# Kernel optimization log

Measured on AMD Instinct MI355X. Metric: run time of the kernel, lower is better.

The kernel has to match this reference:

```python
import jax, jax.numpy as jnp
import numpy as np

N = 100000   # nodes
E = 1600000  # edges
C = 128      # hidden_channels
L = 3        # num_layers
V = 128      # embedding vocab


def setup_inputs() -> dict:
    key = jax.random.key(0)
    ks = jax.random.split(key, 10)
    s = 1.0 / np.sqrt(C)
    return {
        "x_idx": jax.random.randint(ks[0], (N,), 0, V),
        "edge_index": jax.random.randint(ks[1], (2, E), 0, N),
        "edge_weight": jax.random.uniform(ks[2], (E,), dtype=jnp.float32),
        "emb": jax.random.normal(ks[3], (V, C), dtype=jnp.float32),
        "conv_w": jax.random.uniform(ks[4], (L, C, C), minval=-s, maxval=s, dtype=jnp.float32),
        "conv_b": jnp.zeros((L, C), dtype=jnp.float32),
        "lin1_w": jax.random.uniform(ks[5], (C, C), minval=-s, maxval=s, dtype=jnp.float32),
        "lin1_b": jnp.zeros((C,), dtype=jnp.float32),
        "lin2_w": jax.random.uniform(ks[6], (C, 2), minval=-s, maxval=s, dtype=jnp.float32),
        "lin2_b": jnp.zeros((2,), dtype=jnp.float32),
    }


def reference(x_idx, edge_index, edge_weight, emb, conv_w, conv_b,
              lin1_w, lin1_b, lin2_w, lin2_b):
    # GCNConv (PyG): add self-loops (weight 1), symmetric normalization
    row, col = edge_index[0], edge_index[1]
    loop = jnp.arange(N)
    r = jnp.concatenate([row, loop])
    c = jnp.concatenate([col, loop])
    w = jnp.concatenate([edge_weight, jnp.ones((N,), edge_weight.dtype)])
    deg = jax.ops.segment_sum(w, c, num_segments=N)            # [N]
    dinv = jnp.where(deg > 0, jax.lax.rsqrt(deg), 0.0)
    norm = dinv[r] * w * dinv[c]                               # [E+N]

    x = emb[x_idx]                                             # [N, C]
    for i in range(L):
        xw = x @ conv_w[i]                                     # [N, C]
        # message: norm * xw[src], aggregate at dst
        x = jax.ops.segment_sum(norm[:, None] * xw[r], c, num_segments=N) + conv_b[i]
        if i < L - 1:
            x = jax.nn.relu(x)  # dropout is identity in eval mode

    x = jax.nn.relu(x @ lin1_w + lin1_b)
    return x @ lin2_w + lin2_b                                 # [N, 2]
```

## Files before the change

kernel.cpp:

```cpp
#include <hip/hip_runtime.h>
#include <hip/hip_fp16.h>

#define NN 100000
#define NE 1600000
#define CC 128
#define NB_SCAN 391
#define CAP 1900032

typedef _Float16 f16x8 __attribute__((ext_vector_type(8)));
typedef float    f32x4 __attribute__((ext_vector_type(4)));

__global__ void k_init(int* cnt) {
    int i = blockIdx.x * 256 + threadIdx.x;
    if (i < NN) cnt[i] = 0;
}

__global__ void k_count(const int* __restrict__ ei, int* cnt, int* loc) {
    int e = blockIdx.x * 256 + threadIdx.x;
    if (e < NE) {
        int c = ei[NE + e];
        loc[e] = atomicAdd(&cnt[c], 1);
    }
}

__global__ void k_scan1(const int* __restrict__ cnt, int* rowptr, int* bsum) {
    __shared__ int s[256];
    int t = threadIdx.x;
    int i = blockIdx.x * 256 + t;
    int v = (i < NN) ? ((cnt[i] + 3) & ~3) : 0;
    s[t] = v; __syncthreads();
    for (int off = 1; off < 256; off <<= 1) {
        int x = (t >= off) ? s[t - off] : 0;
        __syncthreads();
        s[t] += x;
        __syncthreads();
    }
    if (i < NN) rowptr[i] = s[t] - v;
    if (t == 255) bsum[blockIdx.x] = s[255];
}

__global__ void k_scan2(const int* __restrict__ bsum, int* boff) {
    __shared__ int s[512];
    int t = threadIdx.x;
    int v = (t < NB_SCAN) ? bsum[t] : 0;
    s[t] = v; __syncthreads();
    for (int off = 1; off < 512; off <<= 1) {
        int x = (t >= off) ? s[t - off] : 0;
        __syncthreads();
        s[t] += x;
        __syncthreads();
    }
    if (t < NB_SCAN) boff[t] = s[t] - v;
}

__global__ void k_scan3(int* rowptr, const int* __restrict__ boff,
                        const int* __restrict__ cnt) {
    int i = blockIdx.x * 256 + threadIdx.x;
    if (i < NN) {
        rowptr[i] += boff[i >> 8];
        if (i == NN - 1) rowptr[NN] = rowptr[i] + ((cnt[i] + 3) & ~3);
    }
}

__global__ void k_scatter(const int* __restrict__ ei, const float* __restrict__ ew,
                          const int* __restrict__ loc, const int* __restrict__ rowptr,
                          int2* __restrict__ csr) {
    int e = blockIdx.x * 256 + threadIdx.x;
    if (e < NE) {
        int c = ei[NE + e];
        int pos = rowptr[c] + loc[e];
        csr[pos] = make_int2(ei[e], __float_as_int(ew[e]));
    }
}

__global__ void k_degdinv(const int* __restrict__ rowptr, const int2* __restrict__ csr,
                          float* __restrict__ dinv) {
    int v = blockIdx.x * 256 + threadIdx.x;
    if (v < NN) {
        int b = rowptr[v], e = rowptr[v + 1];
        float s = 1.f;
        for (int i = b; i < e; i++) s += __int_as_float(csr[i].y);
        dinv[v] = rsqrtf(s);
    }
}

__global__ void k_mkcsr0(const int2* __restrict__ csr, const int* __restrict__ xidx,
                         const float* __restrict__ dinv, int2* __restrict__ csr0) {
    int e = blockIdx.x * 256 + threadIdx.x;
    if (e < CAP) {
        int2 c = csr[e];
        csr0[e] = make_int2(xidx[c.x],
                            __float_as_int(__int_as_float(c.y) * dinv[c.x]));
    }
}

__global__ void k_wcvt(const float* __restrict__ conv_w, const float* __restrict__ lin1_w,
                       _Float16* __restrict__ wt) {
    int t = blockIdx.x * 256 + threadIdx.x;
    int l = t >> 14, r = t & 16383;
    int j = r >> 7, k = r & 127;
    const float* src = (l < 2) ? (conv_w + (l + 1) * 16384) : lin1_w;
    wt[l * 16384 + j * 128 + k] = (_Float16)src[k * 128 + j];
}

__global__ void k_embw(const float* __restrict__ emb, const float* __restrict__ w0,
                       __half2* __restrict__ ewh) {
    int t = blockIdx.x * 256 + threadIdx.x;
    int i = t >> 6, jp = t & 63;
    int j0 = jp * 2;
    float a0 = 0.f, a1 = 0.f;
    for (int k = 0; k < 128; k++) {
        float e = emb[i * 128 + k];
        a0 = fmaf(e, w0[k * 128 + j0], a0);
        a1 = fmaf(e, w0[k * 128 + j0 + 1], a1);
    }
    ewh[t] = __floats2half2_rn(a0, a1);
}

template <int SELF_TABLE, int RELU>
__device__ __forceinline__ void agg_core(const _Float16* __restrict__ src16,
                                         const int2* __restrict__ csr,
                                         const int* __restrict__ rowptr,
                                         const int* __restrict__ xidx,
                                         const float* __restrict__ dinv,
                                         const float* __restrict__ bias,
                                         _Float16* __restrict__ xout) {
    int wave = threadIdx.x >> 6, lane = threadIdx.x & 63;
    int g = lane >> 4, sub = lane & 15;
    int v = blockIdx.x * 4 + wave;
    if (v >= NN) return;
    int beg = rowptr[v], end = rowptr[v + 1];
    float acc[8];
#pragma unroll
    for (int i = 0; i < 8; i++) acc[i] = 0.f;
    int e = beg;
    while (e + 8 <= end) {
        int2 c0 = csr[e + g];
        int2 c1 = csr[e + 4 + g];
        f16x8 t0 = *reinterpret_cast<const f16x8*>(&src16[(size_t)c0.x * 128 + sub * 8]);
        f16x8 t1 = *reinterpret_cast<const f16x8*>(&src16[(size_t)c1.x * 128 + sub * 8]);
        float w0 = __int_as_float(c0.y), w1 = __int_as_float(c1.y);
#pragma unroll
        for (int i = 0; i < 8; i++) acc[i] = fmaf(w0, (float)t0[i], acc[i]);
#pragma unroll
        for (int i = 0; i < 8; i++) acc[i] = fmaf(w1, (float)t1[i], acc[i]);
        e += 8;
    }
    if (e < end) {
        int2 c0 = csr[e + g];
        f16x8 t0 = *reinterpret_cast<const f16x8*>(&src16[(size_t)c0.x * 128 + sub * 8]);
        float w0 = __int_as_float(c0.y);
#pragma unroll
        for (int i = 0; i < 8; i++) acc[i] = fmaf(w0, (float)t0[i], acc[i]);
    }
#pragma unroll
    for (int i = 0; i < 8; i++) {
        acc[i] += __shfl_down(acc[i], 32);
        acc[i] += __shfl_down(acc[i], 16);
    }
    if (g == 0) {
        float dv = dinv[v];
        size_t selfoff = SELF_TABLE ? (size_t)xidx[v] * 128 : (size_t)v * 128;
        f16x8 sf = *reinterpret_cast<const f16x8*>(&src16[selfoff + sub * 8]);
        float4 b0 = reinterpret_cast<const float4*>(bias)[sub * 2];
        float4 b1 = reinterpret_cast<const float4*>(bias)[sub * 2 + 1];
        float bb[8] = {b0.x, b0.y, b0.z, b0.w, b1.x, b1.y, b1.z, b1.w};
        f16x8 o;
#pragma unroll
        for (int i = 0; i < 8; i++) {
            float self = SELF_TABLE ? dv * (float)sf[i] : (float)sf[i];
            float r = fmaf(dv, acc[i] + self, bb[i]);
            if (RELU) r = fmaxf(r, 0.f);
            o[i] = (_Float16)r;
        }
        *reinterpret_cast<f16x8*>(&xout[(size_t)v * 128 + sub * 8]) = o;
    }
}

__global__ void k_agg0(const int2* __restrict__ csr0, const int* __restrict__ rowptr,
                       const int* __restrict__ xidx, const float* __restrict__ dinv,
                       const _Float16* __restrict__ ewh, const float* __restrict__ bias,
                       _Float16* __restrict__ xout) {
    agg_core<1, 1>(ewh, csr0, rowptr, xidx, dinv, bias, xout);
}

__global__ void k_agg_r(const _Float16* __restrict__ y, const int* __restrict__ rowptr,
                        const int2* __restrict__ csr, const float* __restrict__ dinv,
                        const float* __restrict__ bias, _Float16* __restrict__ xout) {
    agg_core<0, 1>(y, csr, rowptr, nullptr, dinv, bias, xout);
}

__global__ void k_agg_n(const _Float16* __restrict__ y, const int* __restrict__ rowptr,
                        const int2* __restrict__ csr, const float* __restrict__ dinv,
                        const float* __restrict__ bias, _Float16* __restrict__ xout) {
    agg_core<0, 0>(y, csr, rowptr, nullptr, dinv, bias, xout);
}

template <int MODE>
__global__ __launch_bounds__(256) void k_mgemm(const _Float16* __restrict__ A,
                                               const _Float16* __restrict__ Wt,
                                               const float* __restrict__ dinv,
                                               const float* __restrict__ bias,
                                               _Float16* __restrict__ yout,
                                               const float* __restrict__ w2,
                                               const float* __restrict__ b2,
                                               float* __restrict__ outf) {
    int wid = threadIdx.x >> 6, lane = threadIdx.x & 63;
    int lc = lane & 15, lg = lane >> 4;
    int arow = blockIdx.x * 64 + wid * 16 + lc;
    bool rok = arow < NN;

    f32x4 acc[8];
#pragma unroll
    for (int j = 0; j < 8; j++) acc[j] = (f32x4){0.f, 0.f, 0.f, 0.f};

#pragma unroll
    for (int kc = 0; kc < 4; kc++) {
        int k0 = kc * 32 + lg * 8;
        f16x8 a = {0, 0, 0, 0, 0, 0, 0, 0};
        if (rok) a = *reinterpret_cast<const f16x8*>(&A[arow * 128 + k0]);
#pragma unroll
        for (int j = 0; j < 8; j++) {
            f16x8 b = *reinterpret_cast<const f16x8*>(&Wt[(j * 16 + lc) * 128 + k0]);
            acc[j] = __builtin_amdgcn_mfma_f32_16x16x32_f16(a, b, acc[j], 0, 0, 0);
        }
    }

    int orow0 = blockIdx.x * 64 + wid * 16 + lg * 4;
    if (MODE == 0) {
        float dv[4];
#pragma unroll
        for (int r = 0; r < 4; r++)
            dv[r] = (orow0 + r < NN) ? dinv[orow0 + r] : 0.f;
#pragma unroll
        for (int j = 0; j < 8; j++) {
#pragma unroll
            for (int r = 0; r < 4; r++) {
                int orow = orow0 + r;
                if (orow < NN)
                    yout[orow * 128 + j * 16 + lc] = (_Float16)(dv[r] * acc[j][r]);
            }
        }
    } else {
        float bj[8], w0j[8], w1j[8];
#pragma unroll
        for (int j = 0; j < 8; j++) {
            int c = j * 16 + lc;
            bj[j] = bias[c];
            w0j[j] = w2[c * 2 + 0];
            w1j[j] = w2[c * 2 + 1];
        }
        float bb0 = b2[0], bb1 = b2[1];
#pragma unroll
        for (int r = 0; r < 4; r++) {
            float p0 = 0.f, p1 = 0.f;
#pragma unroll
            for (int j = 0; j < 8; j++) {
                float h = fmaxf(acc[j][r] + bj[j], 0.f);
                p0 = fmaf(h, w0j[j], p0);
                p1 = fmaf(h, w1j[j], p1);
            }
#pragma unroll
            for (int m = 1; m < 16; m <<= 1) {
                p0 += __shfl_xor(p0, m);
                p1 += __shfl_xor(p1, m);
            }
            int orow = orow0 + r;
            if (lc == 0 && orow < NN)
                *reinterpret_cast<float2*>(&outf[orow * 2]) =
                    make_float2(p0 + bb0, p1 + bb1);
        }
    }
}

extern "C" void kernel_launch(void* const* d_in, const int* in_sizes, int n_in,
                              void* d_out, int out_size, void* d_ws, size_t ws_size,
                              hipStream_t stream) {
    const int*   x_idx  = (const int*)d_in[0];
    const int*   ei     = (const int*)d_in[1];
    const float* ew     = (const float*)d_in[2];
    const float* emb    = (const float*)d_in[3];
    const float* conv_w = (const float*)d_in[4];
    const float* conv_b = (const float*)d_in[5];
    const float* lin1_w = (const float*)d_in[6];
    const float* lin1_b = (const float*)d_in[7];
    const float* lin2_w = (const float*)d_in[8];
    const float* lin2_b = (const float*)d_in[9];
    float* out = (float*)d_out;

    char* ws = (char*)d_ws;
    size_t off = 0;
    auto alloc = [&](size_t bytes) -> void* {
        void* p = ws + off;
        off += (bytes + 255) & ~(size_t)255;
        return p;
    };
    float*    dinv   = (float*)alloc(NN * 4);
    int*      cnt    = (int*)alloc(NN * 4);
    int*      rowptr = (int*)alloc((NN + 1) * 4);
    int*      bsum   = (int*)alloc(512 * 4);
    int*      boff   = (int*)alloc(512 * 4);
    int*      loc    = (int*)alloc((size_t)NE * 4);
    int2*     csr    = (int2*)alloc((size_t)CAP * 8);
    int2*     csr0   = (int2*)alloc((size_t)CAP * 8);
    _Float16* ewh    = (_Float16*)alloc(128 * 128 * 2);
    _Float16* wt     = (_Float16*)alloc(3 * 128 * 128 * 2);
    _Float16* xbuf   = (_Float16*)alloc((size_t)NN * CC * 2);
    _Float16* ybuf   = (_Float16*)alloc((size_t)NN * CC * 2);
    (void)ws_size;

    const int NBn = (NN + 255) / 256;
    const int NBe = (NE + 255) / 256;
    const int NBc = CAP / 256;
    const int NBg = (NN + 63) / 64;

    hipMemsetAsync(csr, 0, (size_t)CAP * 8, stream);
    k_init<<<NBn, 256, 0, stream>>>(cnt);
    k_count<<<NBe, 256, 0, stream>>>(ei, cnt, loc);
    k_scan1<<<NB_SCAN, 256, 0, stream>>>(cnt, rowptr, bsum);
    k_scan2<<<1, 512, 0, stream>>>(bsum, boff);
    k_scan3<<<NBn, 256, 0, stream>>>(rowptr, boff, cnt);
    k_scatter<<<NBe, 256, 0, stream>>>(ei, ew, loc, rowptr, csr);
    k_degdinv<<<NBn, 256, 0, stream>>>(rowptr, csr, dinv);
    k_mkcsr0<<<NBc, 256, 0, stream>>>(csr, x_idx, dinv, csr0);
    k_wcvt<<<192, 256, 0, stream>>>(conv_w, lin1_w, wt);

    k_embw<<<32, 256, 0, stream>>>(emb, conv_w, (__half2*)ewh);
    k_agg0<<<NN / 4, 256, 0, stream>>>(csr0, rowptr, x_idx, dinv, ewh,
                                       conv_b + 0 * CC, xbuf);
    k_mgemm<0><<<NBg, 256, 0, stream>>>(xbuf, wt + 0 * 16384, dinv, nullptr, ybuf,
                                        nullptr, nullptr, nullptr);
    k_agg_r<<<NN / 4, 256, 0, stream>>>(ybuf, rowptr, csr, dinv, conv_b + 1 * CC, xbuf);
    k_mgemm<0><<<NBg, 256, 0, stream>>>(xbuf, wt + 1 * 16384, dinv, nullptr, ybuf,
                                        nullptr, nullptr, nullptr);
    k_agg_n<<<NN / 4, 256, 0, stream>>>(ybuf, rowptr, csr, dinv, conv_b + 2 * CC, xbuf);
    k_mgemm<1><<<NBg, 256, 0, stream>>>(xbuf, wt + 2 * 16384, dinv, lin1_b, nullptr,
                                        lin2_w, lin2_b, out);
}
```

Before: 432.9 us.

## Build CSR with two-level binned counting sort in shared memory

Replaces the global-atomic per-node count plus scatter CSR build with a two-pass binned sort. Edges are first histogrammed into 128-node bins per block, then scattered into bin-contiguous buffers, and finally locally sorted in shared memory per bin, which also computes rowptr and dinv. Because rows are no longer padded to multiples of 4, the aggregation tail loop now handles partial groups with masked loads. This removes the memset, the global atomics and the separate degree pass, at the cost of extra intermediate buffers and a reliance on each bin fitting within MAXB shared-memory entries.

```diff
diff --git a/kernel.cpp b/kernel.cpp
--- a/kernel.cpp
+++ b/kernel.cpp
@@ -4,30 +4,36 @@
 #define NN 100000
 #define NE 1600000
 #define CC 128
-#define NB_SCAN 391
-#define CAP 1900032
+#define NBIN 782
+#define BPW 128
+#define MAXB 2560
+#define NHB 256
+#define EPB 6250
 
 typedef _Float16 f16x8 __attribute__((ext_vector_type(8)));
 typedef float    f32x4 __attribute__((ext_vector_type(4)));
 
-__global__ void k_init(int* cnt) {
-    int i = blockIdx.x * 256 + threadIdx.x;
-    if (i < NN) cnt[i] = 0;
-}
-
-__global__ void k_count(const int* __restrict__ ei, int* cnt, int* loc) {
-    int e = blockIdx.x * 256 + threadIdx.x;
-    if (e < NE) {
-        int c = ei[NE + e];
-        loc[e] = atomicAdd(&cnt[c], 1);
-    }
-}
-
-__global__ void k_scan1(const int* __restrict__ cnt, int* rowptr, int* bsum) {
+__global__ __launch_bounds__(256) void k_hist(const int* __restrict__ ei,
+                                              int* __restrict__ hist) {
+    __shared__ int h[NBIN];
+    for (int i = threadIdx.x; i < NBIN; i += 256) h[i] = 0;
+    __syncthreads();
+    int base = blockIdx.x * EPB;
+    for (int i = threadIdx.x; i < EPB; i += 256) {
+        int d = ei[NE + base + i];
+        atomicAdd(&h[d >> 7], 1);
+    }
+    __syncthreads();
+    for (int i = threadIdx.x; i < NBIN; i += 256)
+        hist[blockIdx.x * NBIN + i] = h[i];
+}
+
+__global__ __launch_bounds__(256) void k_scanA(const int* __restrict__ hist,
+                                               int* __restrict__ blockBase,
+                                               int* __restrict__ binTotal) {
     __shared__ int s[256];
-    int t = threadIdx.x;
-    int i = blockIdx.x * 256 + t;
-    int v = (i < NN) ? ((cnt[i] + 3) & ~3) : 0;
+    int bin = blockIdx.x, t = threadIdx.x;
+    int v = hist[t * NBIN + bin];
     s[t] = v; __syncthreads();
     for (int off = 1; off < 256; off <<= 1) {
         int x = (t >= off) ? s[t - off] : 0;
@@ -35,59 +41,103 @@
         s[t] += x;
         __syncthreads();
     }
-    if (i < NN) rowptr[i] = s[t] - v;
-    if (t == 255) bsum[blockIdx.x] = s[255];
-}
-
-__global__ void k_scan2(const int* __restrict__ bsum, int* boff) {
-    __shared__ int s[512];
+    blockBase[t * NBIN + bin] = s[t] - v;
+    if (t == 255) binTotal[bin] = s[255];
+}
+
+__global__ __launch_bounds__(1024) void k_scanB(const int* __restrict__ binTotal,
+                                                int* __restrict__ binStart) {
+    __shared__ int s[1024];
     int t = threadIdx.x;
-    int v = (t < NB_SCAN) ? bsum[t] : 0;
+    int v = (t < NBIN) ? binTotal[t] : 0;
     s[t] = v; __syncthreads();
-    for (int off = 1; off < 512; off <<= 1) {
+    for (int off = 1; off < 1024; off <<= 1) {
         int x = (t >= off) ? s[t - off] : 0;
         __syncthreads();
         s[t] += x;
         __syncthreads();
     }
-    if (t < NB_SCAN) boff[t] = s[t] - v;
-}
-
-__global__ void k_scan3(int* rowptr, const int* __restrict__ boff,
-                        const int* __restrict__ cnt) {
-    int i = blockIdx.x * 256 + threadIdx.x;
-    if (i < NN) {
-        rowptr[i] += boff[i >> 8];
-        if (i == NN - 1) rowptr[NN] = rowptr[i] + ((cnt[i] + 3) & ~3);
-    }
-}
-
-__global__ void k_scatter(const int* __restrict__ ei, const float* __restrict__ ew,
-                          const int* __restrict__ loc, const int* __restrict__ rowptr,
-                          int2* __restrict__ csr) {
-    int e = blockIdx.x * 256 + threadIdx.x;
-    if (e < NE) {
-        int c = ei[NE + e];
-        int pos = rowptr[c] + loc[e];
-        csr[pos] = make_int2(ei[e], __float_as_int(ew[e]));
-    }
-}
-
-__global__ void k_degdinv(const int* __restrict__ rowptr, const int2* __restrict__ csr,
-                          float* __restrict__ dinv) {
-    int v = blockIdx.x * 256 + threadIdx.x;
-    if (v < NN) {
-        int b = rowptr[v], e = rowptr[v + 1];
-        float s = 1.f;
-        for (int i = b; i < e; i++) s += __int_as_float(csr[i].y);
-        dinv[v] = rsqrtf(s);
-    }
+    if (t < NBIN) binStart[t] = s[t] - v;
+    if (t == 1023) binStart[NBIN] = s[1023];
+}
+
+__global__ __launch_bounds__(256) void k_pass2(const int* __restrict__ ei,
+                                               const float* __restrict__ ew,
+                                               const int* __restrict__ binStart,
+                                               const int* __restrict__ blockBase,
+                                               int2* __restrict__ pay,
+                                               unsigned char* __restrict__ key) {
+    __shared__ int cur[NBIN];
+    int blk = blockIdx.x;
+    for (int i = threadIdx.x; i < NBIN; i += 256)
+        cur[i] = binStart[i] + blockBase[blk * NBIN + i];
+    __syncthreads();
+    int base = blk * EPB;
+    for (int i = threadIdx.x; i < EPB; i += 256) {
+        int e = base + i;
+        int d = ei[NE + e];
+        int src = ei[e];
+        float w = ew[e];
+        int pos = atomicAdd(&cur[d >> 7], 1);
+        pay[pos] = make_int2(src, __float_as_int(w));
+        key[pos] = (unsigned char)(d & 127);
+    }
+}
+
+__global__ __launch_bounds__(256) void k_pass3(const int* __restrict__ binStart,
+                                               const int2* __restrict__ pay,
+                                               const unsigned char* __restrict__ key,
+                                               int2* __restrict__ csr,
+                                               int* __restrict__ rowptr,
+                                               float* __restrict__ dinv) {
+    __shared__ int2 sp[MAXB];
+    __shared__ unsigned char sk[MAXB];
+    __shared__ int hist[BPW], excl[BPW], cur[BPW];
+    __shared__ float degw[BPW];
+    int b = blockIdx.x, t = threadIdx.x;
+    int s0 = binStart[b], s1 = binStart[b + 1];
+    int n = s1 - s0;
+    if (t < BPW) { hist[t] = 0; degw[t] = 0.f; }
+    __syncthreads();
+    for (int i = t; i < n; i += 256) {
+        int2 p = pay[s0 + i];
+        unsigned char k = key[s0 + i];
+        sp[i] = p; sk[i] = k;
+        atomicAdd(&hist[k], 1);
+    }
+    __syncthreads();
+    if (t < BPW) excl[t] = hist[t];
+    __syncthreads();
+    for (int off = 1; off < BPW; off <<= 1) {
+        int x = (t < BPW && t >= off) ? excl[t - off] : 0;
+        __syncthreads();
+        if (t < BPW) excl[t] += x;
+        __syncthreads();
+    }
+    if (t < BPW) {
+        int ex = excl[t] - hist[t];
+        excl[t] = ex;
+        cur[t] = ex;
+    }
+    __syncthreads();
+    int node0 = b * BPW;
+    if (t < BPW && node0 + t < NN) rowptr[node0 + t] = s0 + excl[t];
+    if (b == NBIN - 1 && t == 0) rowptr[NN] = NE;
+    for (int i = t; i < n; i += 256) {
+        int2 p = sp[i];
+        unsigned char k = sk[i];
+        int pos = atomicAdd(&cur[k], 1);
+        csr[s0 + pos] = p;
+        atomicAdd(&degw[k], __int_as_float(p.y));
+    }
+    __syncthreads();
+    if (t < BPW && node0 + t < NN) dinv[node0 + t] = rsqrtf(1.f + degw[t]);
 }
 
 __global__ void k_mkcsr0(const int2* __restrict__ csr, const int* __restrict__ xidx,
                          const float* __restrict__ dinv, int2* __restrict__ csr0) {
     int e = blockIdx.x * 256 + threadIdx.x;
-    if (e < CAP) {
+    if (e < NE) {
         int2 c = csr[e];
         csr0[e] = make_int2(xidx[c.x],
                             __float_as_int(__int_as_float(c.y) * dinv[c.x]));
@@ -146,10 +196,12 @@
         for (int i = 0; i < 8; i++) acc[i] = fmaf(w1, (float)t1[i], acc[i]);
         e += 8;
     }
-    if (e < end) {
-        int2 c0 = csr[e + g];
+    for (; e < end; e += 4) {
+        int idx = e + g;
+        bool ok = idx < end;
+        int2 c0 = csr[ok ? idx : beg];
+        float w0 = ok ? __int_as_float(c0.y) : 0.f;
         f16x8 t0 = *reinterpret_cast<const f16x8*>(&src16[(size_t)c0.x * 128 + sub * 8]);
-        float w0 = __int_as_float(c0.y);
 #pragma unroll
         for (int i = 0; i < 8; i++) acc[i] = fmaf(w0, (float)t0[i], acc[i]);
     }
@@ -295,34 +347,31 @@
         off += (bytes + 255) & ~(size_t)255;
         return p;
     };
-    float*    dinv   = (float*)alloc(NN * 4);
-    int*      cnt    = (int*)alloc(NN * 4);
-    int*      rowptr = (int*)alloc((NN + 1) * 4);
-    int*      bsum   = (int*)alloc(512 * 4);
-    int*      boff   = (int*)alloc(512 * 4);
-    int*      loc    = (int*)alloc((size_t)NE * 4);
-    int2*     csr    = (int2*)alloc((size_t)CAP * 8);
-    int2*     csr0   = (int2*)alloc((size_t)CAP * 8);
-    _Float16* ewh    = (_Float16*)alloc(128 * 128 * 2);
-    _Float16* wt     = (_Float16*)alloc(3 * 128 * 128 * 2);
-    _Float16* xbuf   = (_Float16*)alloc((size_t)NN * CC * 2);
-    _Float16* ybuf   = (_Float16*)alloc((size_t)NN * CC * 2);
+    float*         dinv      = (float*)alloc(NN * 4);
+    int*           rowptr    = (int*)alloc((NN + 1) * 4);
+    int*           hist      = (int*)alloc((size_t)NHB * NBIN * 4);
+    int*           blockBase = (int*)alloc((size_t)NHB * NBIN * 4);
+    int*           binTotal  = (int*)alloc(NBIN * 4);
+    int*           binStart  = (int*)alloc((NBIN + 1) * 4);
+    int2*          pay       = (int2*)alloc((size_t)NE * 8);
+    unsigned char* key       = (unsigned char*)alloc(NE);
+    int2*          csr       = (int2*)alloc((size_t)NE * 8);
+    int2*          csr0      = (int2*)alloc((size_t)NE * 8);
+    _Float16*      ewh       = (_Float16*)alloc(128 * 128 * 2);
+    _Float16*      wt        = (_Float16*)alloc(3 * 128 * 128 * 2);
+    _Float16*      xbuf      = (_Float16*)alloc((size_t)NN * CC * 2);
+    _Float16*      ybuf      = (_Float16*)alloc((size_t)NN * CC * 2);
     (void)ws_size;
 
-    const int NBn = (NN + 255) / 256;
     const int NBe = (NE + 255) / 256;
-    const int NBc = CAP / 256;
     const int NBg = (NN + 63) / 64;
 
-    hipMemsetAsync(csr, 0, (size_t)CAP * 8, stream);
-    k_init<<<NBn, 256, 0, stream>>>(cnt);
-    k_count<<<NBe, 256, 0, stream>>>(ei, cnt, loc);
-    k_scan1<<<NB_SCAN, 256, 0, stream>>>(cnt, rowptr, bsum);
-    k_scan2<<<1, 512, 0, stream>>>(bsum, boff);
-    k_scan3<<<NBn, 256, 0, stream>>>(rowptr, boff, cnt);
-    k_scatter<<<NBe, 256, 0, stream>>>(ei, ew, loc, rowptr, csr);
-    k_degdinv<<<NBn, 256, 0, stream>>>(rowptr, csr, dinv);
-    k_mkcsr0<<<NBc, 256, 0, stream>>>(csr, x_idx, dinv, csr0);
+    k_hist<<<NHB, 256, 0, stream>>>(ei, hist);
+    k_scanA<<<NBIN, 256, 0, stream>>>(hist, blockBase, binTotal);
+    k_scanB<<<1, 1024, 0, stream>>>(binTotal, binStart);
+    k_pass2<<<NHB, 256, 0, stream>>>(ei, ew, binStart, blockBase, pay, key);
+    k_pass3<<<NBIN, 256, 0, stream>>>(binStart, pay, key, csr, rowptr, dinv);
+    k_mkcsr0<<<NBe, 256, 0, stream>>>(csr, x_idx, dinv, csr0);
     k_wcvt<<<192, 256, 0, stream>>>(conv_w, lin1_w, wt);
 
     k_embw<<<32, 256, 0, stream>>>(emb, conv_w, (__half2*)ewh);
```

Measured after the change: 390.6 us (median of 2 runs). 1.11x faster.
